# Optimization experiments

Hardware: AMD Instinct MI355X
Metric: run time of the kernel (lower is better)

## Reference

```python
import jax, jax.numpy as jnp
import numpy as np

N = 200000      # total nodes
D = 256         # input_dim
H = 256         # hidden_dim
O = 256         # output_dim
G = 1024        # n_graphs


def setup_inputs() -> dict:
    key = jax.random.key(0)
    ks = jax.random.split(key, 8)
    w = lambda k, shp, fan: jax.random.normal(k, shp, jnp.float32) / np.sqrt(fan)
    # evenly partitioned, sorted segment ids -> every graph non-empty
    batch = ((jnp.arange(N) * G) // N).astype(jnp.int32)
    return {
        "node_features": jax.random.normal(ks[0], (N, D), jnp.float32),
        "batch": batch,
        "num_segments": G,
        "W1": w(ks[1], (D, H), D), "b1": jnp.zeros((H,), jnp.float32),
        "W2": w(ks[2], (H, H), H), "b2": jnp.zeros((H,), jnp.float32),
        "W3": w(ks[3], (H, O), H), "b3": jnp.zeros((O,), jnp.float32),
        "aW1": w(ks[4], (D, H), D), "ab1": jnp.zeros((H,), jnp.float32),
        "aW2": w(ks[5], (H, 1), H), "ab2": jnp.zeros((1,), jnp.float32),
    }


def reference(node_features, batch, num_segments,
              W1, b1, W2, b2, W3, b3, aW1, ab1, aW2, ab2):
    silu = jax.nn.silu
    # MLP: Linear -> SiLU -> Linear -> SiLU -> Linear
    h = silu(node_features @ W1 + b1)
    h = silu(h @ W2 + b2)
    x = h @ W3 + b3                      # (N, O)
    # attention logits: Linear -> SiLU -> Linear(->1)
    logits = (silu(node_features @ aW1 + ab1) @ aW2 + ab2)[:, 0]  # (N,)
    # per-segment stable softmax via segment max/sum
    m = jax.ops.segment_max(logits, batch, num_segments=num_segments)
    ew = jnp.exp(logits - m[batch])
    denom = jax.ops.segment_sum(ew, batch, num_segments=num_segments)
    weights = ew / denom[batch]          # (N,)
    # weighted segment sum -> (G, O)
    out = jax.ops.segment_sum(x * weights[:, None], batch, num_segments=num_segments)
    return out
```

## Files before the change

### kernel.cpp

```cpp
#include <hip/hip_runtime.h>

#define N_NODES 200000
#define DIM 256
#define G_SEG 1024
#define MT 128
#define LDA 264
#define NT 8
#define KSTEPS 8

typedef __bf16 bf16x8 __attribute__((ext_vector_type(8)));
typedef __bf16 bf16x4v __attribute__((ext_vector_type(4)));
typedef float f32x4 __attribute__((ext_vector_type(4)));
typedef unsigned short us16_t __attribute__((ext_vector_type(16)));
typedef unsigned short us8_t __attribute__((ext_vector_type(8)));
typedef unsigned short us4_t __attribute__((ext_vector_type(4)));

__device__ __forceinline__ unsigned short f2bf(float f) {
  unsigned int u = __float_as_uint(f);
  u = u + 0x7FFFu + ((u >> 16) & 1u);
  return (unsigned short)(u >> 16);
}

__device__ __forceinline__ bf16x8 ld_frag(const unsigned short* p) {
  us8_t r = *(const us8_t*)p;
  return __builtin_bit_cast(bf16x8, r);
}

__device__ __forceinline__ float silu(float v) {
  return v * __builtin_amdgcn_rcpf(1.f + __expf(-v));
}

__device__ __forceinline__ void st_bf4(unsigned short* dst, f32x4 x) {
  *(bf16x4v*)dst = __builtin_convertvector(x, bf16x4v);
}

__device__ __forceinline__ void stage_x(const float* __restrict__ X,
                                        unsigned short* A, int base, int tid) {
  #pragma unroll 4
  for (int i = 0; i < 32; ++i) {
    int flat = i * 256 + tid;
    int row = flat >> 6;
    int c4 = flat & 63;
    int grow = base + row;
    float4 v = make_float4(0.f, 0.f, 0.f, 0.f);
    if (grow < N_NODES) v = *(const float4*)(X + (size_t)grow * DIM + c4 * 4);
    f32x4 f = {v.x, v.y, v.z, v.w};
    st_bf4(A + row * LDA + c4 * 4, f);
  }
}

__device__ __forceinline__ void gemm_k256_T(const unsigned short* __restrict__ wlane,
                                            const unsigned short* alane,
                                            f32x4 acc[NT][4]) {
  bf16x8 wcur[4], wnxt[4];
  #pragma unroll
  for (int u = 0; u < 4; ++u) wcur[u] = ld_frag(wlane + u * 512);
  #pragma unroll
  for (int ks = 0; ks < KSTEPS; ++ks) {
    if (ks + 1 < KSTEPS) {
      #pragma unroll
      for (int u = 0; u < 4; ++u)
        wnxt[u] = ld_frag(wlane + ((ks + 1) * 4 + u) * 512);
    }
    #pragma unroll
    for (int t = 0; t < NT; ++t) {
      bf16x8 xfr = ld_frag(alane + t * 16 * LDA + ks * 32);
      #pragma unroll
      for (int u = 0; u < 4; ++u)
        acc[t][u] = __builtin_amdgcn_mfma_f32_16x16x32_bf16(wcur[u], xfr, acc[t][u], 0, 0, 0);
    }
    #pragma unroll
    for (int u = 0; u < 4; ++u) wcur[u] = wnxt[u];
  }
}

__device__ __forceinline__ void zero_acc(f32x4 acc[NT][4]) {
  #pragma unroll
  for (int t = 0; t < NT; ++t)
    #pragma unroll
    for (int u = 0; u < 4; ++u)
      acc[t][u] = (f32x4){0.f, 0.f, 0.f, 0.f};
}

__global__ __launch_bounds__(256) void k_prep(
    const float* __restrict__ W1, const float* __restrict__ W2,
    const float* __restrict__ W3, const float* __restrict__ aW1,
    unsigned short* __restrict__ Wb1, unsigned short* __restrict__ Wb2,
    unsigned short* __restrict__ Wb3, unsigned short* __restrict__ aWb1,
    float* __restrict__ out, float* __restrict__ denom) {
  __shared__ float tlds[64][257];
  int b = blockIdx.x, tid = threadIdx.x;
  if (b < 1024) {
    out[b * 256 + tid] = 0.f;
    return;
  }
  if (b == 1024) {
    #pragma unroll
    for (int i = 0; i < 4; ++i) denom[tid * 4 + i] = 0.f;
    return;
  }
  int bb = b - 1025;
  int mat = bb >> 2, kc = bb & 3, k0 = kc * 64;
  const float* W = (mat == 0) ? W1 : (mat == 1) ? W2 : (mat == 2) ? W3 : aW1;
  unsigned short* Wb = (mat == 0) ? Wb1 : (mat == 1) ? Wb2 : (mat == 2) ? Wb3 : aWb1;
  #pragma unroll 8
  for (int i = 0; i < 64; ++i)
    tlds[i][tid] = W[(size_t)(k0 + i) * 256 + tid];
  __syncthreads();
  #pragma unroll
  for (int i = 0; i < 8; ++i) {
    int idx = i * 256 + tid;
    int lane = idx & 63;
    int u = (idx >> 6) & 3;
    int ksl = (idx >> 8) & 1;
    int wv = idx >> 9;
    int quad = lane >> 4, l15 = lane & 15;
    int row = wv * 64 + u * 16 + l15;
    int ks = kc * 2 + ksl;
    us8_t v;
    #pragma unroll
    for (int j = 0; j < 8; ++j)
      v[j] = f2bf(tlds[ksl * 32 + quad * 8 + j][row]);
    *(us8_t*)(Wb + (size_t)(((wv * 8 + ks) * 4 + u) * 512 + lane * 8)) = v;
  }
}

__global__ __launch_bounds__(256, 2) void k_fused(
    const float* __restrict__ X, const int* __restrict__ batch,
    const unsigned short* __restrict__ aWb1, const float* __restrict__ ab1,
    const float* __restrict__ aW2, const float* __restrict__ ab2,
    const unsigned short* __restrict__ Wb1, const float* __restrict__ b1,
    const unsigned short* __restrict__ Wb2, const float* __restrict__ b2,
    const unsigned short* __restrict__ Wb3, const float* __restrict__ b3,
    float* __restrict__ out, float* __restrict__ denom) {
  __shared__ unsigned short a_lds[MT * LDA];
  __shared__ float l_lds[MT];
  __shared__ float ew0[MT], ew1[MT];
  __shared__ float seg_lds[2];
  int tid = threadIdx.x;
  int base = blockIdx.x * MT;
  stage_x(X, a_lds, base, tid);
  if (tid < MT) l_lds[tid] = 0.f;
  if (tid < 2) seg_lds[tid] = 0.f;
  __syncthreads();

  int wave = tid >> 6, lane = tid & 63, quad = lane >> 4, l15 = lane & 15;
  int wcol0 = wave * 64;
  int fq = wcol0 + quad * 4;
  const unsigned short* alane = a_lds + l15 * LDA + quad * 8;
  unsigned short* elane = a_lds + l15 * LDA + fq;
  int wfoff = wave * 16384 + lane * 8;
  f32x4 acc[NT][4];

  zero_acc(acc);
  gemm_k256_T(aWb1 + wfoff, alane, acc);
  {
    float4 ab1c[4], aw2c[4];
    #pragma unroll
    for (int u = 0; u < 4; ++u) {
      ab1c[u] = *(const float4*)(ab1 + fq + u * 16);
      aw2c[u] = *(const float4*)(aW2 + fq + u * 16);
    }
    #pragma unroll
    for (int t = 0; t < NT; ++t) {
      float p = 0.f;
      #pragma unroll
      for (int u = 0; u < 4; ++u) {
        const float* bb = (const float*)&ab1c[u];
        const float* ww = (const float*)&aw2c[u];
        #pragma unroll
        for (int r = 0; r < 4; ++r)
          p += silu(acc[t][u][r] + bb[r]) * ww[r];
      }
      p += __shfl_xor(p, 16); p += __shfl_xor(p, 32);
      if (quad == 0) atomicAdd(&l_lds[t * 16 + l15], p);
    }
  }

  zero_acc(acc);
  gemm_k256_T(Wb1 + wfoff, alane, acc);
  __syncthreads();
  if (tid < MT) {
    int grow = base + tid;
    float e = 0.f; int ds = 0;
    if (grow < N_NODES) {
      e = __expf(l_lds[tid] + ab2[0]);
      ds = batch[grow] - batch[base];
    }
    ew0[tid] = ds ? 0.f : e;
    ew1[tid] = ds ? e : 0.f;
    if (e != 0.f) atomicAdd(&seg_lds[ds], e);
  }
  {
    float4 bc[4];
    #pragma unroll
    for (int u = 0; u < 4; ++u) bc[u] = *(const float4*)(b1 + fq + u * 16);
    #pragma unroll
    for (int t = 0; t < NT; ++t)
      #pragma unroll
      for (int u = 0; u < 4; ++u) {
        const float* bb = (const float*)&bc[u];
        f32x4 h;
        #pragma unroll
        for (int r = 0; r < 4; ++r)
          h[r] = silu(acc[t][u][r] + bb[r]);
        st_bf4(elane + t * 16 * LDA + u * 16, h);
      }
  }
  __syncthreads();

  zero_acc(acc);
  gemm_k256_T(Wb2 + wfoff, alane, acc);
  __syncthreads();
  {
    float4 bc[4];
    #pragma unroll
    for (int u = 0; u < 4; ++u) bc[u] = *(const float4*)(b2 + fq + u * 16);
    #pragma unroll
    for (int t = 0; t < NT; ++t)
      #pragma unroll
      for (int u = 0; u < 4; ++u) {
        const float* bb = (const float*)&bc[u];
        f32x4 h;
        #pragma unroll
        for (int r = 0; r < 4; ++r)
          h[r] = silu(acc[t][u][r] + bb[r]);
        st_bf4(elane + t * 16 * LDA + u * 16, h);
      }
  }
  __syncthreads();

  zero_acc(acc);
  gemm_k256_T(Wb3 + wfoff, alane, acc);
  {
    float4 bc[4];
    #pragma unroll
    for (int u = 0; u < 4; ++u) bc[u] = *(const float4*)(b3 + fq + u * 16);
    float s0a[4][4], s1a[4][4];
    #pragma unroll
    for (int u = 0; u < 4; ++u)
      #pragma unroll
      for (int r = 0; r < 4; ++r) { s0a[u][r] = 0.f; s1a[u][r] = 0.f; }
    #pragma unroll
    for (int t = 0; t < NT; ++t) {
      float w0 = ew0[t * 16 + l15];
      float w1 = ew1[t * 16 + l15];
      #pragma unroll
      for (int u = 0; u < 4; ++u) {
        const float* bb = (const float*)&bc[u];
        #pragma unroll
        for (int r = 0; r < 4; ++r) {
          float x = acc[t][u][r] + bb[r];
          s0a[u][r] += x * w0;
          s1a[u][r] += x * w1;
        }
      }
    }
    int s0 = batch[base];
    #pragma unroll
    for (int u = 0; u < 4; ++u)
      #pragma unroll
      for (int r = 0; r < 4; ++r) {
        float a0 = s0a[u][r];
        a0 += __shfl_xor(a0, 1); a0 += __shfl_xor(a0, 2);
        a0 += __shfl_xor(a0, 4); a0 += __shfl_xor(a0, 8);
        float a1 = s1a[u][r];
        a1 += __shfl_xor(a1, 1); a1 += __shfl_xor(a1, 2);
        a1 += __shfl_xor(a1, 4); a1 += __shfl_xor(a1, 8);
        if (l15 == 0) {
          int col = fq + u * 16 + r;
          atomicAdd(&out[(size_t)s0 * 256 + col], a0);
          if (s0 + 1 < G_SEG && a1 != 0.f)
            atomicAdd(&out[(size_t)(s0 + 1) * 256 + col], a1);
        }
      }
    if (tid < 2) {
      float v = seg_lds[tid];
      if (v != 0.f) atomicAdd(&denom[s0 + tid], v);
    }
  }
}

__global__ __launch_bounds__(256) void k_final(float* __restrict__ out,
                                               const float* __restrict__ denom) {
  int b = blockIdx.x, tid = threadIdx.x;
  out[b * 256 + tid] *= __builtin_amdgcn_rcpf(denom[b]);
}

extern "C" void kernel_launch(void* const* d_in, const int* in_sizes, int n_in,
                              void* d_out, int out_size, void* d_ws, size_t ws_size,
                              hipStream_t stream) {
  const float* X    = (const float*)d_in[0];
  const int* batch  = (const int*)d_in[1];
  const float* W1  = (const float*)d_in[3];
  const float* b1  = (const float*)d_in[4];
  const float* W2  = (const float*)d_in[5];
  const float* b2  = (const float*)d_in[6];
  const float* W3  = (const float*)d_in[7];
  const float* b3  = (const float*)d_in[8];
  const float* aW1 = (const float*)d_in[9];
  const float* ab1 = (const float*)d_in[10];
  const float* aW2 = (const float*)d_in[11];
  const float* ab2 = (const float*)d_in[12];
  float* out = (float*)d_out;

  char* ws = (char*)d_ws;
  unsigned short* Wb1  = (unsigned short*)(ws);
  unsigned short* Wb2  = (unsigned short*)(ws + 131072);
  unsigned short* Wb3  = (unsigned short*)(ws + 262144);
  unsigned short* aWb1 = (unsigned short*)(ws + 393216);
  float* denom = (float*)(ws + 524288);

  hipLaunchKernelGGL(k_prep, dim3(1041), dim3(256), 0, stream,
                     W1, W2, W3, aW1, Wb1, Wb2, Wb3, aWb1, out, denom);
  int nblk = (N_NODES + MT - 1) / MT;
  hipLaunchKernelGGL(k_fused, dim3(nblk), dim3(256), 0, stream,
                     X, batch, aWb1, ab1, aW2, ab2,
                     Wb1, b1, Wb2, b2, Wb3, b3, out, denom);
  hipLaunchKernelGGL(k_final, dim3(G_SEG), dim3(256), 0, stream, out, denom);
}
```

Before: 440.7 us.

## Double wave count per block, halve per-wave N tile, fold b3 into finalize

The fused kernel now runs 512 threads (8 waves), each covering 32 output columns instead of 64, which halves the accumulator registers per wave and targets higher occupancy. The weight-fragment prefetch becomes a three-deep ring buffer, X staging gets a bounds-check-free fast path, and the b3 bias is moved out of the per-node accumulation into k_final, since the softmax weights sum to one per segment. The prep kernel zeroes the output with float4 stores using fewer blocks. The trade-off is that each wave now reloads the A fragments from LDS for only half as many MFMAs.

New measurement: 398.9 us. 1.1x faster.

```diff
diff --git a/kernel.cpp b/kernel.cpp
--- a/kernel.cpp
+++ b/kernel.cpp
@@ -6,7 +6,9 @@
 #define MT 128
 #define LDA 264
 #define NT 8
+#define NU 2
 #define KSTEPS 8
+#define THREADS 512
 
 typedef __bf16 bf16x8 __attribute__((ext_vector_type(8)));
 typedef __bf16 bf16x4v __attribute__((ext_vector_type(4)));
@@ -36,49 +38,61 @@
 
 __device__ __forceinline__ void stage_x(const float* __restrict__ X,
                                         unsigned short* A, int base, int tid) {
-  #pragma unroll 4
-  for (int i = 0; i < 32; ++i) {
-    int flat = i * 256 + tid;
-    int row = flat >> 6;
-    int c4 = flat & 63;
-    int grow = base + row;
-    float4 v = make_float4(0.f, 0.f, 0.f, 0.f);
-    if (grow < N_NODES) v = *(const float4*)(X + (size_t)grow * DIM + c4 * 4);
-    f32x4 f = {v.x, v.y, v.z, v.w};
-    st_bf4(A + row * LDA + c4 * 4, f);
+  if (base + MT <= N_NODES) {
+    #pragma unroll 4
+    for (int i = 0; i < 16; ++i) {
+      int flat = i * THREADS + tid;
+      int row = flat >> 6;
+      int c4 = flat & 63;
+      float4 v = *(const float4*)(X + (size_t)(base + row) * DIM + c4 * 4);
+      f32x4 f = {v.x, v.y, v.z, v.w};
+      st_bf4(A + row * LDA + c4 * 4, f);
+    }
+  } else {
+    #pragma unroll 4
+    for (int i = 0; i < 16; ++i) {
+      int flat = i * THREADS + tid;
+      int row = flat >> 6;
+      int c4 = flat & 63;
+      float4 v = make_float4(0.f, 0.f, 0.f, 0.f);
+      if (base + row < N_NODES)
+        v = *(const float4*)(X + (size_t)(base + row) * DIM + c4 * 4);
+      f32x4 f = {v.x, v.y, v.z, v.w};
+      st_bf4(A + row * LDA + c4 * 4, f);
+    }
   }
 }
 
 __device__ __forceinline__ void gemm_k256_T(const unsigned short* __restrict__ wlane,
                                             const unsigned short* alane,
-                                            f32x4 acc[NT][4]) {
-  bf16x8 wcur[4], wnxt[4];
-  #pragma unroll
-  for (int u = 0; u < 4; ++u) wcur[u] = ld_frag(wlane + u * 512);
+                                            f32x4 acc[NT][NU]) {
+  bf16x8 wb[3][NU];
+  #pragma unroll
+  for (int u = 0; u < NU; ++u) wb[0][u] = ld_frag(wlane + u * 512);
+  #pragma unroll
+  for (int u = 0; u < NU; ++u) wb[1][u] = ld_frag(wlane + (4 + u) * 512);
   #pragma unroll
   for (int ks = 0; ks < KSTEPS; ++ks) {
-    if (ks + 1 < KSTEPS) {
-      #pragma unroll
-      for (int u = 0; u < 4; ++u)
-        wnxt[u] = ld_frag(wlane + ((ks + 1) * 4 + u) * 512);
+    if (ks + 2 < KSTEPS) {
+      #pragma unroll
+      for (int u = 0; u < NU; ++u)
+        wb[(ks + 2) % 3][u] = ld_frag(wlane + ((ks + 2) * 4 + u) * 512);
     }
     #pragma unroll
     for (int t = 0; t < NT; ++t) {
       bf16x8 xfr = ld_frag(alane + t * 16 * LDA + ks * 32);
       #pragma unroll
-      for (int u = 0; u < 4; ++u)
-        acc[t][u] = __builtin_amdgcn_mfma_f32_16x16x32_bf16(wcur[u], xfr, acc[t][u], 0, 0, 0);
-    }
-    #pragma unroll
-    for (int u = 0; u < 4; ++u) wcur[u] = wnxt[u];
-  }
-}
-
-__device__ __forceinline__ void zero_acc(f32x4 acc[NT][4]) {
+      for (int u = 0; u < NU; ++u)
+        acc[t][u] = __builtin_amdgcn_mfma_f32_16x16x32_bf16(wb[ks % 3][u], xfr, acc[t][u], 0, 0, 0);
+    }
+  }
+}
+
+__device__ __forceinline__ void zero_acc(f32x4 acc[NT][NU]) {
   #pragma unroll
   for (int t = 0; t < NT; ++t)
     #pragma unroll
-    for (int u = 0; u < 4; ++u)
+    for (int u = 0; u < NU; ++u)
       acc[t][u] = (f32x4){0.f, 0.f, 0.f, 0.f};
 }
 
@@ -90,16 +104,19 @@
     float* __restrict__ out, float* __restrict__ denom) {
   __shared__ float tlds[64][257];
   int b = blockIdx.x, tid = threadIdx.x;
-  if (b < 1024) {
-    out[b * 256 + tid] = 0.f;
+  if (b < 64) {
+    float4* o4 = (float4*)out;
+    #pragma unroll
+    for (int j = 0; j < 4; ++j)
+      o4[b * 1024 + j * 256 + tid] = make_float4(0.f, 0.f, 0.f, 0.f);
     return;
   }
-  if (b == 1024) {
+  if (b == 64) {
     #pragma unroll
     for (int i = 0; i < 4; ++i) denom[tid * 4 + i] = 0.f;
     return;
   }
-  int bb = b - 1025;
+  int bb = b - 65;
   int mat = bb >> 2, kc = bb & 3, k0 = kc * 64;
   const float* W = (mat == 0) ? W1 : (mat == 1) ? W2 : (mat == 2) ? W3 : aW1;
   unsigned short* Wb = (mat == 0) ? Wb1 : (mat == 1) ? Wb2 : (mat == 2) ? Wb3 : aWb1;
@@ -125,13 +142,13 @@
   }
 }
 
-__global__ __launch_bounds__(256, 2) void k_fused(
+__global__ __launch_bounds__(THREADS, 4) void k_fused(
     const float* __restrict__ X, const int* __restrict__ batch,
     const unsigned short* __restrict__ aWb1, const float* __restrict__ ab1,
     const float* __restrict__ aW2, const float* __restrict__ ab2,
     const unsigned short* __restrict__ Wb1, const float* __restrict__ b1,
     const unsigned short* __restrict__ Wb2, const float* __restrict__ b2,
-    const unsigned short* __restrict__ Wb3, const float* __restrict__ b3,
+    const unsigned short* __restrict__ Wb3,
     float* __restrict__ out, float* __restrict__ denom) {
   __shared__ unsigned short a_lds[MT * LDA];
   __shared__ float l_lds[MT];
@@ -145,19 +162,19 @@
   __syncthreads();
 
   int wave = tid >> 6, lane = tid & 63, quad = lane >> 4, l15 = lane & 15;
-  int wcol0 = wave * 64;
+  int wcol0 = wave * 32;
   int fq = wcol0 + quad * 4;
   const unsigned short* alane = a_lds + l15 * LDA + quad * 8;
   unsigned short* elane = a_lds + l15 * LDA + fq;
-  int wfoff = wave * 16384 + lane * 8;
-  f32x4 acc[NT][4];
+  int wfoff = (wave >> 1) * 16384 + (wave & 1) * 1024 + lane * 8;
+  f32x4 acc[NT][NU];
 
   zero_acc(acc);
   gemm_k256_T(aWb1 + wfoff, alane, acc);
   {
-    float4 ab1c[4], aw2c[4];
-    #pragma unroll
-    for (int u = 0; u < 4; ++u) {
+    float4 ab1c[NU], aw2c[NU];
+    #pragma unroll
+    for (int u = 0; u < NU; ++u) {
       ab1c[u] = *(const float4*)(ab1 + fq + u * 16);
       aw2c[u] = *(const float4*)(aW2 + fq + u * 16);
     }
@@ -165,7 +182,7 @@
     for (int t = 0; t < NT; ++t) {
       float p = 0.f;
       #pragma unroll
-      for (int u = 0; u < 4; ++u) {
+      for (int u = 0; u < NU; ++u) {
         const float* bb = (const float*)&ab1c[u];
         const float* ww = (const float*)&aw2c[u];
         #pragma unroll
@@ -192,13 +209,13 @@
     if (e != 0.f) atomicAdd(&seg_lds[ds], e);
   }
   {
-    float4 bc[4];
-    #pragma unroll
-    for (int u = 0; u < 4; ++u) bc[u] = *(const float4*)(b1 + fq + u * 16);
+    float4 bc[NU];
+    #pragma unroll
+    for (int u = 0; u < NU; ++u) bc[u] = *(const float4*)(b1 + fq + u * 16);
     #pragma unroll
     for (int t = 0; t < NT; ++t)
       #pragma unroll
-      for (int u = 0; u < 4; ++u) {
+      for (int u = 0; u < NU; ++u) {
         const float* bb = (const float*)&bc[u];
         f32x4 h;
         #pragma unroll
@@ -213,13 +230,13 @@
   gemm_k256_T(Wb2 + wfoff, alane, acc);
   __syncthreads();
   {
-    float4 bc[4];
-    #pragma unroll
-    for (int u = 0; u < 4; ++u) bc[u] = *(const float4*)(b2 + fq + u * 16);
+    float4 bc[NU];
+    #pragma unroll
+    for (int u = 0; u < NU; ++u) bc[u] = *(const float4*)(b2 + fq + u * 16);
     #pragma unroll
     for (int t = 0; t < NT; ++t)
       #pragma unroll
-      for (int u = 0; u < 4; ++u) {
+      for (int u = 0; u < NU; ++u) {
         const float* bb = (const float*)&bc[u];
         f32x4 h;
         #pragma unroll
@@ -233,12 +250,9 @@
   zero_acc(acc);
   gemm_k256_T(Wb3 + wfoff, alane, acc);
   {
-    float4 bc[4];
-    #pragma unroll
-    for (int u = 0; u < 4; ++u) bc[u] = *(const float4*)(b3 + fq + u * 16);
-    float s0a[4][4], s1a[4][4];
-    #pragma unroll
-    for (int u = 0; u < 4; ++u)
+    float s0a[NU][4], s1a[NU][4];
+    #pragma unroll
+    for (int u = 0; u < NU; ++u)
       #pragma unroll
       for (int r = 0; r < 4; ++r) { s0a[u][r] = 0.f; s1a[u][r] = 0.f; }
     #pragma unroll
@@ -246,19 +260,17 @@
       float w0 = ew0[t * 16 + l15];
       float w1 = ew1[t * 16 + l15];
       #pragma unroll
-      for (int u = 0; u < 4; ++u) {
-        const float* bb = (const float*)&bc[u];
+      for (int u = 0; u < NU; ++u)
         #pragma unroll
         for (int r = 0; r < 4; ++r) {
-          float x = acc[t][u][r] + bb[r];
+          float x = acc[t][u][r];
           s0a[u][r] += x * w0;
           s1a[u][r] += x * w1;
         }
-      }
     }
     int s0 = batch[base];
     #pragma unroll
-    for (int u = 0; u < 4; ++u)
+    for (int u = 0; u < NU; ++u)
       #pragma unroll
       for (int r = 0; r < 4; ++r) {
         float a0 = s0a[u][r];
@@ -282,9 +294,10 @@
 }
 
 __global__ __launch_bounds__(256) void k_final(float* __restrict__ out,
-                                               const float* __restrict__ denom) {
+                                               const float* __restrict__ denom,
+                                               const float* __restrict__ b3) {
   int b = blockIdx.x, tid = threadIdx.x;
-  out[b * 256 + tid] *= __builtin_amdgcn_rcpf(denom[b]);
+  out[b * 256 + tid] = out[b * 256 + tid] * __builtin_amdgcn_rcpf(denom[b]) + b3[tid];
 }
 
 extern "C" void kernel_launch(void* const* d_in, const int* in_sizes, int n_in,
@@ -311,11 +324,11 @@
   unsigned short* aWb1 = (unsigned short*)(ws + 393216);
   float* denom = (float*)(ws + 524288);
 
-  hipLaunchKernelGGL(k_prep, dim3(1041), dim3(256), 0, stream,
+  hipLaunchKernelGGL(k_prep, dim3(81), dim3(256), 0, stream,
                      W1, W2, W3, aW1, Wb1, Wb2, Wb3, aWb1, out, denom);
   int nblk = (N_NODES + MT - 1) / MT;
-  hipLaunchKernelGGL(k_fused, dim3(nblk), dim3(256), 0, stream,
+  hipLaunchKernelGGL(k_fused, dim3(nblk), dim3(THREADS), 0, stream,
                      X, batch, aWb1, ab1, aW2, ab2,
-                     Wb1, b1, Wb2, b2, Wb3, b3, out, denom);
-  hipLaunchKernelGGL(k_final, dim3(G_SEG), dim3(256), 0, stream, out, denom);
-}
+                     Wb1, b1, Wb2, b2, Wb3, out, denom);
+  hipLaunchKernelGGL(k_final, dim3(G_SEG), dim3(256), 0, stream, out, denom, b3);
+}
```
